# Kernel optimization log

Hardware: AMD Instinct MI355X
Metric: run time of the kernel (lower is better)

## Reference

```python
import jax, jax.numpy as jnp
import numpy as np


def setup_inputs() -> dict:
    key = jax.random.key(0)
    ks = jax.random.split(key, 4)
    B, T, E, H = 4, 4096, 512, 64
    x = jax.random.normal(ks[0], (B, T, E), dtype=jnp.float32)
    s = 1.0 / np.sqrt(E)
    Wq = jax.random.normal(ks[1], (E, H), dtype=jnp.float32) * s
    Wk = jax.random.normal(ks[2], (E, H), dtype=jnp.float32) * s
    Wv = jax.random.normal(ks[3], (E, H), dtype=jnp.float32) * s
    bq = jnp.zeros((H,), dtype=jnp.float32)
    bk = jnp.zeros((H,), dtype=jnp.float32)
    bv = jnp.zeros((H,), dtype=jnp.float32)
    return {"x": x, "Wq": Wq, "bq": bq, "Wk": Wk, "bk": bk, "Wv": Wv, "bv": bv}


def reference(x, Wq, bq, Wk, bk, Wv, bv):
    # Single-head causal attention (masked=True path; dropout off / eval mode).
    B, T, E = x.shape
    H = Wq.shape[1]
    q = x @ Wq + bq                      # [B,T,H]
    k = x @ Wk + bk                      # [B,T,H]
    v = x @ Wv + bv                      # [B,T,H]
    scale = jnp.asarray(H, x.dtype) ** -0.5
    w = jnp.einsum('bqh,bkh->bqk', q, k) * scale   # [B,T,T]
    causal = jnp.tril(jnp.ones((T, T), dtype=bool))
    w = jnp.where(causal, w, jnp.asarray(-jnp.inf, w.dtype))
    w = jax.nn.softmax(w, axis=-1)
    out = jnp.einsum('bqk,bkh->bqh', w, v)          # [B,T,H]
    return out
```

## Files before the change

### kernel.cpp

```cpp
#include <hip/hip_runtime.h>
#include <math.h>

#define B_SZ   4
#define T_SEQ  4096
#define E_DIM  512
#define H_DIM  64
#define AW     8
#define XSTR   520
#define QSCALE 0.180336878f

typedef float f32x4 __attribute__((ext_vector_type(4)));
typedef short s16x4 __attribute__((ext_vector_type(4)));
typedef short s16x8 __attribute__((ext_vector_type(8)));
typedef unsigned int u32x4 __attribute__((ext_vector_type(4)));

static __device__ __forceinline__ unsigned short f2bf(float f) {
    union { float f; unsigned int u; } c; c.f = f;
    return (unsigned short)((c.u + 0x7fffu + ((c.u >> 16) & 1u)) >> 16);
}

static __device__ __forceinline__ float exp2f_hw(float x) {
    return __builtin_amdgcn_exp2f(x);
}

static __device__ __forceinline__ unsigned int pack_bf16(float a, float b) {
    unsigned int ua = __builtin_bit_cast(unsigned int, a) + 0x8000u;
    unsigned int ub = __builtin_bit_cast(unsigned int, b) + 0x8000u;
    return __builtin_amdgcn_perm(ub, ua, 0x07060302u);
}

__global__ __launch_bounds__(256) void wconv(
    const float* __restrict__ Wq, const float* __restrict__ Wk, const float* __restrict__ Wv,
    unsigned short* __restrict__ Wf)
{
    const int fid  = blockIdx.x * 256 + threadIdx.x;
    const int nt   = fid >> 10;
    const int kc32 = (fid >> 6) & 15;
    const int lane = fid & 63;
    const int l15  = lane & 15, g = lane >> 4;
    const int col  = nt * 16 + l15;
    const int m    = col >> 6, h = col & 63;
    const float* src = (m == 0) ? Wq : (m == 1) ? Wk : Wv;
    const float sc = (m == 0) ? QSCALE : 1.0f;
    const int k0 = kc32 * 32 + 4 * g;
    s16x8 o;
    #pragma unroll
    for (int j = 0; j < 4; ++j) {
        o[j]     = (short)f2bf(src[(k0 + j) * H_DIM + h] * sc);
        o[4 + j] = (short)f2bf(src[(k0 + 16 + j) * H_DIM + h] * sc);
    }
    *(s16x8*)(Wf + (long long)fid * 8) = o;
}

__global__ __launch_bounds__(256) void qkv_mfma(
    const float* __restrict__ x, const unsigned short* __restrict__ Wf,
    const float* __restrict__ bq, const float* __restrict__ bk, const float* __restrict__ bv,
    unsigned short* __restrict__ qf, unsigned short* __restrict__ kf,
    unsigned short* __restrict__ vf)
{
    __shared__ unsigned short Xf[2][16 * XSTR];
    __shared__ unsigned short Wout[192][36];

    const int t = threadIdx.x, wv = t >> 6, l = t & 63, l15 = l & 15, g = l >> 4;
    const long long row0 = (long long)blockIdx.x * 32;

    const float* xbase = x + row0 * E_DIM;
    #pragma unroll
    for (int i = 0; i < 16; ++i) {
        const int n = t + 256 * i;
        const int r = n >> 7;
        const int c = (n & 127) * 4;
        const f32x4 xv = *(const f32x4*)(xbase + r * E_DIM + c);
        const int rs = r >> 4, rr = r & 15;
        const int kc32 = c >> 5, rem = c & 31;
        const int gg = (rem & 15) >> 2, half = rem >> 4;
        unsigned int* dst = (unsigned int*)&Xf[rs][kc32 * XSTR + (rr + 16 * gg) * 8 + half * 4];
        dst[0] = pack_bf16(xv[0], xv[1]);
        dst[1] = pack_bf16(xv[2], xv[3]);
    }
    __syncthreads();

    f32x4 acc[2][3];
    #pragma unroll
    for (int rs = 0; rs < 2; ++rs)
        #pragma unroll
        for (int i = 0; i < 3; ++i) acc[rs][i] = (f32x4){0.f, 0.f, 0.f, 0.f};

    #pragma unroll
    for (int kc32 = 0; kc32 < 16; ++kc32) {
        const s16x8 xf0 = *(const s16x8*)&Xf[0][kc32 * XSTR + l * 8];
        const s16x8 xf1 = *(const s16x8*)&Xf[1][kc32 * XSTR + l * 8];
        #pragma unroll
        for (int i = 0; i < 3; ++i) {
            const int nt = wv + 4 * i;
            const s16x8 wf = *(const s16x8*)(Wf + (long long)((nt * 16 + kc32) * 64 + l) * 8);
            acc[0][i] = __builtin_amdgcn_mfma_f32_16x16x32_bf16(wf, xf0, acc[0][i], 0, 0, 0);
            acc[1][i] = __builtin_amdgcn_mfma_f32_16x16x32_bf16(wf, xf1, acc[1][i], 0, 0, 0);
        }
    }

    #pragma unroll
    for (int i = 0; i < 3; ++i) {
        const int nt = wv + 4 * i;
        const float* bsrc = (i == 0) ? bq : (i == 1) ? bk : bv;
        const float bscale = (i == 0) ? QSCALE : 1.0f;
        const f32x4 bb = *(const f32x4*)(bsrc + wv * 16 + 4 * g);
        #pragma unroll
        for (int rs = 0; rs < 2; ++rs)
            #pragma unroll
            for (int r = 0; r < 4; ++r)
                Wout[nt * 16 + 4 * g + r][16 * rs + l15] = f2bf(acc[rs][i][r] + bb[r] * bscale);
    }
    __syncthreads();

    #pragma unroll
    for (int rt = 0; rt < 2; ++rt) {
        const long long qt = (long long)blockIdx.x * 2 + rt;

        if (t < 128) {
            const int hc = t >> 6, ll = t & 63, p15 = ll & 15, pg = (ll >> 4);
            s16x8 o;
            #pragma unroll
            for (int j = 0; j < 4; ++j) {
                o[j]     = (short)Wout[32 * hc + 4 * pg + j][16 * rt + p15];
                o[4 + j] = (short)Wout[32 * hc + 16 + 4 * pg + j][16 * rt + p15];
            }
            *(s16x8*)(qf + qt * 1024 + hc * 512 + ll * 8) = o;
        } else {
            const int tt = t - 128, half = tt >> 6, ll = tt & 63, p15 = ll & 15, pg = (ll >> 4);
            s16x8 o;
            #pragma unroll
            for (int j = 0; j < 4; ++j) {
                o[j]     = (short)Wout[64 + 32 * half + 4 * pg + j][16 * rt + p15];
                o[4 + j] = (short)Wout[64 + 32 * half + 16 + 4 * pg + j][16 * rt + p15];
            }
            *(s16x8*)(kf + qt * 1024 + half * 512 + ll * 8) = o;
        }

        {
            const int hc = t >> 6, ll = t & 63, p15 = ll & 15, pg = (ll >> 4);
            const long long ktg = qt >> 2;
            const int half = (int)((qt >> 1) & 1), pi = (int)(qt & 1);
            s16x4 o;
            #pragma unroll
            for (int j = 0; j < 4; ++j)
                o[j] = (short)Wout[128 + hc * 16 + p15][16 * rt + 4 * pg + j];
            *(s16x4*)(vf + ktg * 4096 + hc * 1024 + half * 512 + ll * 8 + pi * 4) = o;
        }
    }
}

__global__ __launch_bounds__(512, 1) void attn(
    const unsigned short* __restrict__ qf,
    const unsigned short* __restrict__ kf,
    const unsigned short* __restrict__ vf,
    float* __restrict__ out)
{
    __shared__ float Osh[AW][64][65];
    __shared__ float msh[AW][64];
    __shared__ float lsh[AW][64];

    const int t = threadIdx.x, wv = t >> 6, l = t & 63, l15 = l & 15, g = l >> 4;

    const int bid = blockIdx.x;
    const int xcd = bid & 7;
    const int b   = xcd >> 1;
    const int u   = (bid >> 3) * 2 + (xcd & 1);
    const int qi  = 63 - u;
    const int q0  = qi * 64;
    const int adiag = qi;

    const unsigned short* kfb = kf + (long long)b * 64 * 4096 + l * 8;
    const unsigned short* vfb = vf + (long long)b * 64 * 4096 + l * 8;

    s16x8 Qf[4][2];
    #pragma unroll
    for (int s = 0; s < 4; ++s) {
        const unsigned short* qp = qf + ((long long)b * 256 + qi * 4 + s) * 1024 + l * 8;
        Qf[s][0] = *(const s16x8*)qp;
        Qf[s][1] = *(const s16x8*)(qp + 512);
    }

    f32x4 O[4][4];
    #pragma unroll
    for (int s = 0; s < 4; ++s)
        #pragma unroll
        for (int hc = 0; hc < 4; ++hc) O[s][hc] = (f32x4){0.f, 0.f, 0.f, 0.f};
    float m[4]   = {-INFINITY, -INFINITY, -INFINITY, -INFINITY};
    float lsm[4] = {0.f, 0.f, 0.f, 0.f};

    s16x8 Ka[4], Kc[4];
    #define LOAD_K(KT, A, C)                                              \
        {                                                                 \
            const unsigned short* p_ = kfb + (long long)(KT) * 4096;      \
            _Pragma("unroll")                                             \
            for (int ks = 0; ks < 4; ++ks) {                              \
                (A)[ks] = *(const s16x8*)(p_ + ks * 1024);                \
                (C)[ks] = *(const s16x8*)(p_ + ks * 1024 + 512);          \
            }                                                             \
        }

    if (wv <= adiag) LOAD_K(wv, Ka, Kc);

    for (int kt = wv; kt <= adiag; kt += AW) {
        const int ktb = kt * 64;
        const f32x4 z = {0.f, 0.f, 0.f, 0.f};

        f32x4 S[4][4];
        __builtin_amdgcn_s_setprio(1);
        #pragma unroll
        for (int ks = 0; ks < 4; ++ks) {
            #pragma unroll
            for (int s = 0; s < 4; ++s) {
                f32x4 s0 = __builtin_amdgcn_mfma_f32_16x16x32_bf16(Ka[ks], Qf[s][0], z, 0, 0, 0);
                S[s][ks] = __builtin_amdgcn_mfma_f32_16x16x32_bf16(Kc[ks], Qf[s][1], s0, 0, 0, 0);
            }
        }
        __builtin_amdgcn_s_setprio(0);

        s16x8 Va[4], Vc[4];
        {
            const unsigned short* pv = vfb + (long long)kt * 4096;
            #pragma unroll
            for (int hc = 0; hc < 4; ++hc) {
                Va[hc] = *(const s16x8*)(pv + hc * 1024);
                Vc[hc] = *(const s16x8*)(pv + hc * 1024 + 512);
            }
        }

        s16x8 Kna[4], Knc[4];
        const int ktn = kt + AW;
        if (ktn <= adiag) LOAD_K(ktn, Kna, Knc);

        if (kt == adiag) {
            #pragma unroll
            for (int s = 0; s < 4; ++s) {
                const int qg = q0 + 16 * s + l15;
                #pragma unroll
                for (int ks = 0; ks < 4; ++ks)
                    #pragma unroll
                    for (int r = 0; r < 4; ++r) {
                        const int key = ktb + 16 * ks + 4 * g + r;
                        S[s][ks][r] = (key > qg) ? -INFINITY : S[s][ks][r];
                    }
            }
        }

        s16x8 Pf[4][2];
        #pragma unroll
        for (int s = 0; s < 4; ++s) {
            float tm = S[s][0][0];
            #pragma unroll
            for (int ks = 0; ks < 4; ++ks)
                #pragma unroll
                for (int r = 0; r < 4; ++r) tm = fmaxf(tm, S[s][ks][r]);

            if (!__all(tm - m[s] <= 8.f)) {
                float tr = fmaxf(tm, __shfl_xor(tm, 16));
                tr = fmaxf(tr, __shfl_xor(tr, 32));
                const float mn = fmaxf(m[s], tr);
                const float alpha = exp2f_hw(m[s] - mn);
                lsm[s] *= alpha;
                #pragma unroll
                for (int hc = 0; hc < 4; ++hc) O[s][hc] *= alpha;
                m[s] = mn;
            }

            float ps = 0.f;
            #pragma unroll
            for (int ks = 0; ks < 4; ++ks)
                #pragma unroll
                for (int r = 0; r < 4; ++r) {
                    const float pp = exp2f_hw(S[s][ks][r] - m[s]);
                    S[s][ks][r] = pp;
                    ps += pp;
                }
            lsm[s] += ps;

            #pragma unroll
            for (int kc = 0; kc < 2; ++kc) {
                u32x4 w;
                #pragma unroll
                for (int i = 0; i < 4; ++i)
                    w[i] = pack_bf16(S[s][2 * kc + (i >> 1)][2 * (i & 1)],
                                     S[s][2 * kc + (i >> 1)][2 * (i & 1) + 1]);
                Pf[s][kc] = __builtin_bit_cast(s16x8, w);
            }
        }

        __builtin_amdgcn_s_setprio(1);
        #pragma unroll
        for (int hc = 0; hc < 4; ++hc) {
            #pragma unroll
            for (int s = 0; s < 4; ++s) {
                O[s][hc] = __builtin_amdgcn_mfma_f32_16x16x32_bf16(Va[hc], Pf[s][0], O[s][hc], 0, 0, 0);
                O[s][hc] = __builtin_amdgcn_mfma_f32_16x16x32_bf16(Vc[hc], Pf[s][1], O[s][hc], 0, 0, 0);
            }
        }
        __builtin_amdgcn_s_setprio(0);

        #pragma unroll
        for (int ks = 0; ks < 4; ++ks) { Ka[ks] = Kna[ks]; Kc[ks] = Knc[ks]; }
    }
    #undef LOAD_K

    #pragma unroll
    for (int s = 0; s < 4; ++s) {
        lsm[s] += __shfl_xor(lsm[s], 16);
        lsm[s] += __shfl_xor(lsm[s], 32);
    }

    #pragma unroll
    for (int s = 0; s < 4; ++s)
        #pragma unroll
        for (int hc = 0; hc < 4; ++hc)
            #pragma unroll
            for (int r = 0; r < 4; ++r)
                Osh[wv][hc * 16 + 4 * g + r][16 * s + l15] = O[s][hc][r];
    if (g == 0) {
        #pragma unroll
        for (int s = 0; s < 4; ++s) {
            msh[wv][16 * s + l15] = m[s];
            lsh[wv][16 * s + l15] = lsm[s];
        }
    }
    __syncthreads();

    const int rl = t >> 3;
    const int h0 = (t & 7) * 8;
    float mstar = msh[0][rl];
    #pragma unroll
    for (int w = 1; w < AW; ++w) mstar = fmaxf(mstar, msh[w][rl]);
    float fw[AW], lstar = 0.f;
    #pragma unroll
    for (int w = 0; w < AW; ++w) {
        fw[w] = exp2f_hw(msh[w][rl] - mstar);
        lstar += lsh[w][rl] * fw[w];
    }
    const float inv = 1.f / lstar;

    f32x4 o0, o1;
    #pragma unroll
    for (int j = 0; j < 4; ++j) {
        float a0 = 0.f, a1 = 0.f;
        #pragma unroll
        for (int w = 0; w < AW; ++w) {
            a0 += Osh[w][h0 + j][rl] * fw[w];
            a1 += Osh[w][h0 + 4 + j][rl] * fw[w];
        }
        o0[j] = a0 * inv;
        o1[j] = a1 * inv;
    }
    float* op = out + ((long long)b * T_SEQ + q0 + rl) * H_DIM + h0;
    *(f32x4*)op = o0;
    *(f32x4*)(op + 4) = o1;
}

extern "C" void kernel_launch(void* const* d_in, const int* in_sizes, int n_in,
                              void* d_out, int out_size, void* d_ws, size_t ws_size,
                              hipStream_t stream) {
    const float* x  = (const float*)d_in[0];
    const float* Wq = (const float*)d_in[1];
    const float* bq = (const float*)d_in[2];
    const float* Wk = (const float*)d_in[3];
    const float* bk = (const float*)d_in[4];
    const float* Wv = (const float*)d_in[5];
    const float* bv = (const float*)d_in[6];

    const long long rows = (long long)B_SZ * T_SEQ;
    unsigned short* qfb = (unsigned short*)d_ws;
    unsigned short* kfb = qfb + rows * H_DIM;
    unsigned short* vfb = kfb + rows * H_DIM;
    unsigned short* Wfb = vfb + rows * H_DIM;

    wconv<<<dim3(48), dim3(256), 0, stream>>>(Wq, Wk, Wv, Wfb);
    qkv_mfma<<<dim3(rows / 32), dim3(256), 0, stream>>>(x, Wfb, bq, bk, bv, qfb, kfb, vfb);
    attn<<<dim3(B_SZ * 64), dim3(512), 0, stream>>>(qfb, kfb, vfb, (float*)d_out);
}
```

Measured before the change: 49.16 us.

## Process 64 rows per QKV block and restructure attention loop per query sub-tile

The QKV projection kernel now handles 64 rows per block instead of 32, so each weight fragment loaded from global memory feeds four MFMAs instead of two. This halves the grid and doubles the LDS footprint. In the attention kernel, the next-K prefetch is dropped and K and V are loaded together at the top of each iteration. The S/softmax/PV work is also reorganised to run per 16-row query sub-tile, shrinking the live S and P register sets to reduce register pressure, at the cost of exposing K load latency that the prefetch used to hide.

```diff
diff --git a/kernel.cpp b/kernel.cpp
--- a/kernel.cpp
+++ b/kernel.cpp
@@ -58,15 +58,15 @@
     unsigned short* __restrict__ qf, unsigned short* __restrict__ kf,
     unsigned short* __restrict__ vf)
 {
-    __shared__ unsigned short Xf[2][16 * XSTR];
-    __shared__ unsigned short Wout[192][36];
+    __shared__ unsigned short Xf[4][16 * XSTR];
+    __shared__ unsigned short Wout[192][68];
 
     const int t = threadIdx.x, wv = t >> 6, l = t & 63, l15 = l & 15, g = l >> 4;
-    const long long row0 = (long long)blockIdx.x * 32;
+    const long long row0 = (long long)blockIdx.x * 64;
 
     const float* xbase = x + row0 * E_DIM;
     #pragma unroll
-    for (int i = 0; i < 16; ++i) {
+    for (int i = 0; i < 32; ++i) {
         const int n = t + 256 * i;
         const int r = n >> 7;
         const int c = (n & 127) * 4;
@@ -80,22 +80,25 @@
     }
     __syncthreads();
 
-    f32x4 acc[2][3];
-    #pragma unroll
-    for (int rs = 0; rs < 2; ++rs)
+    f32x4 acc[4][3];
+    #pragma unroll
+    for (int rs = 0; rs < 4; ++rs)
         #pragma unroll
         for (int i = 0; i < 3; ++i) acc[rs][i] = (f32x4){0.f, 0.f, 0.f, 0.f};
 
     #pragma unroll
     for (int kc32 = 0; kc32 < 16; ++kc32) {
-        const s16x8 xf0 = *(const s16x8*)&Xf[0][kc32 * XSTR + l * 8];
-        const s16x8 xf1 = *(const s16x8*)&Xf[1][kc32 * XSTR + l * 8];
+        s16x8 xfv[4];
+        #pragma unroll
+        for (int rs = 0; rs < 4; ++rs)
+            xfv[rs] = *(const s16x8*)&Xf[rs][kc32 * XSTR + l * 8];
         #pragma unroll
         for (int i = 0; i < 3; ++i) {
             const int nt = wv + 4 * i;
             const s16x8 wf = *(const s16x8*)(Wf + (long long)((nt * 16 + kc32) * 64 + l) * 8);
-            acc[0][i] = __builtin_amdgcn_mfma_f32_16x16x32_bf16(wf, xf0, acc[0][i], 0, 0, 0);
-            acc[1][i] = __builtin_amdgcn_mfma_f32_16x16x32_bf16(wf, xf1, acc[1][i], 0, 0, 0);
+            #pragma unroll
+            for (int rs = 0; rs < 4; ++rs)
+                acc[rs][i] = __builtin_amdgcn_mfma_f32_16x16x32_bf16(wf, xfv[rs], acc[rs][i], 0, 0, 0);
         }
     }
 
@@ -106,7 +109,7 @@
         const float bscale = (i == 0) ? QSCALE : 1.0f;
         const f32x4 bb = *(const f32x4*)(bsrc + wv * 16 + 4 * g);
         #pragma unroll
-        for (int rs = 0; rs < 2; ++rs)
+        for (int rs = 0; rs < 4; ++rs)
             #pragma unroll
             for (int r = 0; r < 4; ++r)
                 Wout[nt * 16 + 4 * g + r][16 * rs + l15] = f2bf(acc[rs][i][r] + bb[r] * bscale);
@@ -114,8 +117,8 @@
     __syncthreads();
 
     #pragma unroll
-    for (int rt = 0; rt < 2; ++rt) {
-        const long long qt = (long long)blockIdx.x * 2 + rt;
+    for (int rt = 0; rt < 4; ++rt) {
+        const long long qt = (long long)blockIdx.x * 4 + rt;
 
         if (t < 128) {
             const int hc = t >> 6, ll = t & 63, p15 = ll & 15, pg = (ll >> 4);
@@ -189,71 +192,50 @@
     float m[4]   = {-INFINITY, -INFINITY, -INFINITY, -INFINITY};
     float lsm[4] = {0.f, 0.f, 0.f, 0.f};
 
-    s16x8 Ka[4], Kc[4];
-    #define LOAD_K(KT, A, C)                                              \
-        {                                                                 \
-            const unsigned short* p_ = kfb + (long long)(KT) * 4096;      \
-            _Pragma("unroll")                                             \
-            for (int ks = 0; ks < 4; ++ks) {                              \
-                (A)[ks] = *(const s16x8*)(p_ + ks * 1024);                \
-                (C)[ks] = *(const s16x8*)(p_ + ks * 1024 + 512);          \
-            }                                                             \
-        }
-
-    if (wv <= adiag) LOAD_K(wv, Ka, Kc);
-
     for (int kt = wv; kt <= adiag; kt += AW) {
         const int ktb = kt * 64;
         const f32x4 z = {0.f, 0.f, 0.f, 0.f};
 
-        f32x4 S[4][4];
-        __builtin_amdgcn_s_setprio(1);
-        #pragma unroll
-        for (int ks = 0; ks < 4; ++ks) {
-            #pragma unroll
-            for (int s = 0; s < 4; ++s) {
+        s16x8 Ka[4], Kc[4], Va[4], Vc[4];
+        {
+            const unsigned short* pk = kfb + (long long)kt * 4096;
+            const unsigned short* pv = vfb + (long long)kt * 4096;
+            #pragma unroll
+            for (int ks = 0; ks < 4; ++ks) {
+                Ka[ks] = *(const s16x8*)(pk + ks * 1024);
+                Kc[ks] = *(const s16x8*)(pk + ks * 1024 + 512);
+                Va[ks] = *(const s16x8*)(pv + ks * 1024);
+                Vc[ks] = *(const s16x8*)(pv + ks * 1024 + 512);
+            }
+        }
+
+        #pragma unroll
+        for (int s = 0; s < 4; ++s) {
+            f32x4 S[4];
+            __builtin_amdgcn_s_setprio(1);
+            #pragma unroll
+            for (int ks = 0; ks < 4; ++ks) {
                 f32x4 s0 = __builtin_amdgcn_mfma_f32_16x16x32_bf16(Ka[ks], Qf[s][0], z, 0, 0, 0);
-                S[s][ks] = __builtin_amdgcn_mfma_f32_16x16x32_bf16(Kc[ks], Qf[s][1], s0, 0, 0, 0);
-            }
-        }
-        __builtin_amdgcn_s_setprio(0);
-
-        s16x8 Va[4], Vc[4];
-        {
-            const unsigned short* pv = vfb + (long long)kt * 4096;
-            #pragma unroll
-            for (int hc = 0; hc < 4; ++hc) {
-                Va[hc] = *(const s16x8*)(pv + hc * 1024);
-                Vc[hc] = *(const s16x8*)(pv + hc * 1024 + 512);
-            }
-        }
-
-        s16x8 Kna[4], Knc[4];
-        const int ktn = kt + AW;
-        if (ktn <= adiag) LOAD_K(ktn, Kna, Knc);
-
-        if (kt == adiag) {
-            #pragma unroll
-            for (int s = 0; s < 4; ++s) {
-                const int qg = q0 + 16 * s + l15;
+                S[ks]    = __builtin_amdgcn_mfma_f32_16x16x32_bf16(Kc[ks], Qf[s][1], s0, 0, 0, 0);
+            }
+            __builtin_amdgcn_s_setprio(0);
+
+            if (kt == adiag) {
+                const int qg_row = q0 + 16 * s + l15;
                 #pragma unroll
                 for (int ks = 0; ks < 4; ++ks)
                     #pragma unroll
                     for (int r = 0; r < 4; ++r) {
                         const int key = ktb + 16 * ks + 4 * g + r;
-                        S[s][ks][r] = (key > qg) ? -INFINITY : S[s][ks][r];
+                        S[ks][r] = (key > qg_row) ? -INFINITY : S[ks][r];
                     }
             }
-        }
-
-        s16x8 Pf[4][2];
-        #pragma unroll
-        for (int s = 0; s < 4; ++s) {
-            float tm = S[s][0][0];
+
+            float tm = S[0][0];
             #pragma unroll
             for (int ks = 0; ks < 4; ++ks)
                 #pragma unroll
-                for (int r = 0; r < 4; ++r) tm = fmaxf(tm, S[s][ks][r]);
+                for (int r = 0; r < 4; ++r) tm = fmaxf(tm, S[ks][r]);
 
             if (!__all(tm - m[s] <= 8.f)) {
                 float tr = fmaxf(tm, __shfl_xor(tm, 16));
@@ -271,38 +253,32 @@
             for (int ks = 0; ks < 4; ++ks)
                 #pragma unroll
                 for (int r = 0; r < 4; ++r) {
-                    const float pp = exp2f_hw(S[s][ks][r] - m[s]);
-                    S[s][ks][r] = pp;
+                    const float pp = exp2f_hw(S[ks][r] - m[s]);
+                    S[ks][r] = pp;
                     ps += pp;
                 }
             lsm[s] += ps;
 
+            s16x8 Pf[2];
             #pragma unroll
             for (int kc = 0; kc < 2; ++kc) {
                 u32x4 w;
                 #pragma unroll
                 for (int i = 0; i < 4; ++i)
-                    w[i] = pack_bf16(S[s][2 * kc + (i >> 1)][2 * (i & 1)],
-                                     S[s][2 * kc + (i >> 1)][2 * (i & 1) + 1]);
-                Pf[s][kc] = __builtin_bit_cast(s16x8, w);
-            }
-        }
-
-        __builtin_amdgcn_s_setprio(1);
-        #pragma unroll
-        for (int hc = 0; hc < 4; ++hc) {
-            #pragma unroll
-            for (int s = 0; s < 4; ++s) {
-                O[s][hc] = __builtin_amdgcn_mfma_f32_16x16x32_bf16(Va[hc], Pf[s][0], O[s][hc], 0, 0, 0);
-                O[s][hc] = __builtin_amdgcn_mfma_f32_16x16x32_bf16(Vc[hc], Pf[s][1], O[s][hc], 0, 0, 0);
-            }
-        }
-        __builtin_amdgcn_s_setprio(0);
-
-        #pragma unroll
-        for (int ks = 0; ks < 4; ++ks) { Ka[ks] = Kna[ks]; Kc[ks] = Knc[ks]; }
-    }
-    #undef LOAD_K
+                    w[i] = pack_bf16(S[2 * kc + (i >> 1)][2 * (i & 1)],
+                                     S[2 * kc + (i >> 1)][2 * (i & 1) + 1]);
+                Pf[kc] = __builtin_bit_cast(s16x8, w);
+            }
+
+            __builtin_amdgcn_s_setprio(1);
+            #pragma unroll
+            for (int hc = 0; hc < 4; ++hc) {
+                O[s][hc] = __builtin_amdgcn_mfma_f32_16x16x32_bf16(Va[hc], Pf[0], O[s][hc], 0, 0, 0);
+                O[s][hc] = __builtin_amdgcn_mfma_f32_16x16x32_bf16(Vc[hc], Pf[1], O[s][hc], 0, 0, 0);
+            }
+            __builtin_amdgcn_s_setprio(0);
+        }
+    }
 
     #pragma unroll
     for (int s = 0; s < 4; ++s) {
@@ -374,6 +350,6 @@
     unsigned short* Wfb = vfb + rows * H_DIM;
 
     wconv<<<dim3(48), dim3(256), 0, stream>>>(Wq, Wk, Wv, Wfb);
-    qkv_mfma<<<dim3(rows / 32), dim3(256), 0, stream>>>(x, Wfb, bq, bk, bv, qfb, kfb, vfb);
+    qkv_mfma<<<dim3(rows / 64), dim3(256), 0, stream>>>(x, Wfb, bq, bk, bv, qfb, kfb, vfb);
     attn<<<dim3(B_SZ * 64), dim3(512), 0, stream>>>(qfb, kfb, vfb, (float*)d_out);
 }
```

Result: faster. 47.85 us (-2.7%).
